# Kernel tuning notes

Measured on AMD Instinct MI355X. Metric: run time of the kernel, lower is better.

The kernel has to match this reference:

```python
import jax, jax.numpy as jnp
import numpy as np
from jax.scipy.special import logsumexp

B, T, D, H, BASIS = 16, 512, 256, 8, 8
E = D // H  # att_emb_size = 32
SINKHORN_ITERS = 20


def setup_inputs() -> dict:
    key = jax.random.key(0)
    ks = jax.random.split(key, 9)
    s = 1.0 / np.sqrt(D)
    return {
        'X': jax.random.normal(ks[0], (B, T, D), jnp.float32),
        'token_embeddings': jax.random.normal(ks[1], (T, D), jnp.float32) * s,
        'Wq_meta': jax.random.normal(ks[2], (T, BASIS, D), jnp.float32) * s,
        'Wk_meta': jax.random.normal(ks[3], (T, BASIS, D), jnp.float32) * s,
        'Q_basis': jax.random.normal(ks[4], (BASIS, D, H * E), jnp.float32) * s,
        'K_basis': jax.random.normal(ks[5], (BASIS, D, H * E), jnp.float32) * s,
        'W_V': jax.random.normal(ks[6], (T, D, H * E), jnp.float32) * s,
        'A_logits': jax.random.normal(ks[7], (T, T), jnp.float32) * 0.05,
        'lambda_logits': jax.random.normal(ks[8], (T, T), jnp.float32) * 0.05,
    }


def log_sinkhorn(log_alpha, n_iters=SINKHORN_ITERS):
    def body(i, la):
        la = la - logsumexp(la, axis=-1, keepdims=True)
        la = la - logsumexp(la, axis=-2, keepdims=True)
        return la
    return jnp.exp(jax.lax.fori_loop(0, n_iters, body, log_alpha))


def reference(X, token_embeddings, Wq_meta, Wk_meta, Q_basis, K_basis, W_V, A_logits, lambda_logits):
    # per-token basis mixing weights: Linear(d,basis) applied to token i's embedding
    q_w = jnp.einsum('td,tkd->tk', token_embeddings, Wq_meta)  # [T, basis]
    k_w = jnp.einsum('td,tkd->tk', token_embeddings, Wk_meta)
    Q_tilde = jnp.einsum('tk,kde->tde', q_w, Q_basis)  # [T, D, H*E]
    K_tilde = jnp.einsum('tk,kde->tde', k_w, K_basis)
    querys = jnp.einsum('btd,tde->bte', X, Q_tilde)  # [B, T, H*E]
    keys = jnp.einsum('btd,tde->bte', X, K_tilde)
    values = jnp.einsum('btd,tde->bte', X, W_V)
    # -> [H, B, T, E]
    q = querys.reshape(B, T, H, E).transpose(2, 0, 1, 3)
    k = keys.reshape(B, T, H, E).transpose(2, 0, 1, 3)
    v = values.reshape(B, T, H, E).transpose(2, 0, 1, 3)
    scores = jnp.einsum('hbte,hbse->hbts', q, k) / np.sqrt(E).astype(np.float32)
    att = jax.nn.softmax(scores, axis=-1)  # dropout=0 (eval)
    lam = jax.nn.sigmoid(lambda_logits)  # [T, T]
    A_sym = 0.5 * (A_logits + A_logits.T)
    att = lam[None, None] * A_sym[None, None] + (1.0 - lam)[None, None] * att
    att = 0.5 * (att + jnp.swapaxes(att, -1, -2))
    att = log_sinkhorn(att)
    out = jnp.einsum('hbts,hbse->hbte', att, v)  # [H, B, T, E]
    return out.transpose(1, 2, 0, 3).reshape(B, T, D)
```

## Files before the change

### kernel.cpp

```cpp
#include <hip/hip_runtime.h>
#include <hip/hip_bf16.h>
#include <stdint.h>


#define B_  16
#define T_  512
#define D_  256
#define H_  8
#define E_  32
#define HE_ 256
#define KB_ 8
#define HB_ 128

typedef unsigned short u16;
typedef __attribute__((ext_vector_type(8))) short short8;
typedef __attribute__((ext_vector_type(4))) float floatx4;

__device__ __forceinline__ float bflo(uint32_t u){ return __uint_as_float(u << 16); }
__device__ __forceinline__ float bfhi(uint32_t u){ return __uint_as_float(u & 0xffff0000u); }
__device__ __forceinline__ u16 f2bf(float f){
  uint32_t u = __float_as_uint(f);
  return (u16)((u + 0x7fffu + ((u >> 16) & 1u)) >> 16);
}
__device__ __forceinline__ uint32_t pk2(float a, float b){
  return (uint32_t)f2bf(a) | ((uint32_t)f2bf(b) << 16);
}

__global__ void __launch_bounds__(256)
kcvt_x(const float* __restrict__ X, u16* __restrict__ Xb){
  int idx = (blockIdx.x*256 + threadIdx.x)*4;
  float4 v = *(const float4*)(X + idx);
  uint2 o; o.x = pk2(v.x, v.y); o.y = pk2(v.z, v.w);
  *(uint2*)(Xb + idx) = o;
}

__global__ void __launch_bounds__(256)
kT_basis(const float* __restrict__ Qb, const float* __restrict__ Kb,
         u16* __restrict__ QbT, u16* __restrict__ KbT){
  __shared__ float tile[64][65];
  int slot = blockIdx.y;
  const float* src = (slot < 8) ? Qb + (size_t)slot*D_*HE_ : Kb + (size_t)(slot-8)*D_*HE_;
  u16*         dst = (slot < 8) ? QbT + (size_t)slot*HE_*D_ : KbT + (size_t)(slot-8)*HE_*D_;
  int ti = blockIdx.x >> 2, tj = blockIdx.x & 3;
  int tid = threadIdx.x;
  #pragma unroll
  for (int i = 0; i < 16; ++i){
    int idx = tid + 256*i;
    int rr = idx >> 6, cc = idx & 63;
    tile[rr][cc] = src[(size_t)(ti*64 + rr)*HE_ + tj*64 + cc];
  }
  __syncthreads();
  #pragma unroll
  for (int i = 0; i < 16; ++i){
    int idx = tid + 256*i;
    int rr = idx >> 6, cc = idx & 63;
    dst[(size_t)(tj*64 + rr)*D_ + ti*64 + cc] = f2bf(tile[cc][rr]);
  }
}

__global__ void k0_meta(const float* __restrict__ te, const float* __restrict__ wq,
                        const float* __restrict__ wk, float* __restrict__ qw,
                        float* __restrict__ kw){
  int t = blockIdx.x;
  int lane = threadIdx.x;
  int k = lane >> 3, part = lane & 7;
  const float* ta = te + t*D_ + part*32;
  const float* qa = wq + (t*KB_ + k)*D_ + part*32;
  const float* ka = wk + (t*KB_ + k)*D_ + part*32;
  float sq = 0.f, sk = 0.f;
  #pragma unroll
  for (int i = 0; i < 8; ++i){
    float4 a = ((const float4*)ta)[i];
    float4 b = ((const float4*)qa)[i];
    float4 c = ((const float4*)ka)[i];
    sq += a.x*b.x + a.y*b.y + a.z*b.z + a.w*b.w;
    sk += a.x*c.x + a.y*c.y + a.z*c.z + a.w*c.w;
  }
  sq += __shfl_down(sq, 4, 8); sq += __shfl_down(sq, 2, 8); sq += __shfl_down(sq, 1, 8);
  sk += __shfl_down(sk, 4, 8); sk += __shfl_down(sk, 2, 8); sk += __shfl_down(sk, 1, 8);
  if (part == 0){
    qw[t*KB_ + k] = sq * 0.17677669529663687f;
    kw[t*KB_ + k] = sk;
  }
}

__global__ void __launch_bounds__(256)
k_pre(const float* __restrict__ A, const float* __restrict__ L,
      u16* __restrict__ lA, u16* __restrict__ oml){
  __shared__ float tile[64][65];
  int I = blockIdx.x >> 3, J = blockIdx.x & 7;
  int tid = threadIdx.x;
  #pragma unroll
  for (int i = 0; i < 16; ++i){
    int idx = tid + 256*i;
    int rr = idx >> 6, cc = idx & 63;
    tile[rr][cc] = A[(J*64 + rr)*T_ + I*64 + cc];
  }
  __syncthreads();
  #pragma unroll
  for (int i = 0; i < 16; ++i){
    int idx = tid + 256*i;
    int rr = idx >> 6, cc = idx & 63;
    int t = I*64 + rr, s = J*64 + cc;
    float lamv = 1.0f / (1.0f + __expf(-L[t*T_ + s]));
    float asym = 0.5f*(A[t*T_ + s] + tile[cc][rr]);
    lA[t*T_ + s]  = f2bf(lamv*asym);
    oml[t*T_ + s] = f2bf(1.0f - lamv);
  }
}

__global__ void __launch_bounds__(256)
k1a_gemm(const u16* __restrict__ Xb, const u16* __restrict__ BT, u16* __restrict__ Y){
  __shared__ u16 At[128*40];
  __shared__ u16 Bt[128*40];
  int bt0 = blockIdx.x*128;
  int j   = blockIdx.y;
  int kb  = blockIdx.z;
  const u16* Bsrc = BT + (size_t)kb*HE_*D_;
  int tid = threadIdx.x, lane = tid & 63, w = tid >> 6;
  int q_l = lane >> 4, c_l = lane & 15;
  int srow = tid >> 2, sch = (tid & 3)*8;
  floatx4 acc[2][8];
  #pragma unroll
  for (int mt = 0; mt < 2; ++mt)
    #pragma unroll
    for (int n = 0; n < 8; ++n) acc[mt][n] = (floatx4){0,0,0,0};

  #pragma unroll 1
  for (int ks = 0; ks < 8; ++ks){
    int k0 = ks*32;
    if (ks) __syncthreads();
    *(short8*)&At[srow*40 + sch] = *(const short8*)&Xb[(size_t)(bt0 + srow)*D_ + k0 + sch];
    *(short8*)&Bt[srow*40 + sch] = *(const short8*)&Bsrc[(size_t)(j*128 + srow)*D_ + k0 + sch];
    __syncthreads();
    short8 a0 = *(const short8*)&At[(w*32 +  0 + c_l)*40 + q_l*8];
    short8 a1 = *(const short8*)&At[(w*32 + 16 + c_l)*40 + q_l*8];
    #pragma unroll
    for (int n = 0; n < 8; ++n){
      short8 bfr = *(const short8*)&Bt[(n*16 + c_l)*40 + q_l*8];
      acc[0][n] = __builtin_amdgcn_mfma_f32_16x16x32_bf16(a0, bfr, acc[0][n], 0, 0, 0);
      acc[1][n] = __builtin_amdgcn_mfma_f32_16x16x32_bf16(a1, bfr, acc[1][n], 0, 0, 0);
    }
  }
  #pragma unroll
  for (int mt = 0; mt < 2; ++mt)
    #pragma unroll
    for (int n = 0; n < 8; ++n)
      #pragma unroll
      for (int r = 0; r < 4; ++r){
        int row = w*32 + mt*16 + q_l*4 + r;
        int e = j*128 + n*16 + c_l;
        Y[((size_t)kb << 21) + (size_t)(bt0 + row)*HE_ + e] = f2bf(acc[mt][n][r]);
      }
}

__global__ void __launch_bounds__(256)
k1b_mix(const u16* __restrict__ Y, const float* __restrict__ wv, u16* __restrict__ dst){
  int tid = threadIdx.x;
  int row = blockIdx.x*16 + (tid >> 4);
  int e0 = (tid & 15)*16;
  int b = row >> 9, t = row & 511;
  float w8[8];
  #pragma unroll
  for (int k = 0; k < 8; ++k) w8[k] = wv[t*8 + k];
  float acc[16];
  #pragma unroll
  for (int i = 0; i < 16; ++i) acc[i] = 0.f;
  #pragma unroll
  for (int k = 0; k < 8; ++k){
    const u16* yp = Y + ((size_t)k << 21) + (size_t)row*HE_ + e0;
    uint4 v0 = *(const uint4*)yp;
    uint4 v1 = *(const uint4*)(yp + 8);
    uint32_t vv[8] = {v0.x,v0.y,v0.z,v0.w,v1.x,v1.y,v1.z,v1.w};
    float wk = w8[k];
    #pragma unroll
    for (int d = 0; d < 8; ++d){
      acc[2*d]   += wk*bflo(vv[d]);
      acc[2*d+1] += wk*bfhi(vv[d]);
    }
  }
  uint4 o0, o1;
  o0.x = pk2(acc[0],acc[1]);   o0.y = pk2(acc[2],acc[3]);
  o0.z = pk2(acc[4],acc[5]);   o0.w = pk2(acc[6],acc[7]);
  o1.x = pk2(acc[8],acc[9]);   o1.y = pk2(acc[10],acc[11]);
  o1.z = pk2(acc[12],acc[13]); o1.w = pk2(acc[14],acc[15]);
  int h = e0 >> 5, off = e0 & 31;
  u16* dp = dst + (((size_t)(h*16 + b)*T_ + t)*E_ + off);
  *(uint4*)dp = o0;
  *(uint4*)(dp + 8) = o1;
}

__global__ void __launch_bounds__(512)
k1c_v(const u16* __restrict__ Xb, const float* __restrict__ WV, u16* __restrict__ v_ws){
  __shared__ u16 lds[128*256];
  int t = blockIdx.x;
  int tid = threadIdx.x;
  int d = tid >> 1, esub = (tid & 1)*64;
  int lane = tid & 63, wv = tid >> 6;
  int q_l = lane >> 4, c_l = lane & 15;
  short8 afrag[8];
  #pragma unroll
  for (int kk = 0; kk < 8; ++kk)
    afrag[kk] = *(const short8*)&Xb[((size_t)c_l*T_ + t)*D_ + kk*32 + q_l*8];
  for (int eh = 0; eh < 2; ++eh){
    #pragma unroll 1
    for (int i = 0; i < 8; ++i){
      int el0 = esub + 8*i;
      int eg0 = eh*128 + el0;
      const float* p = &WV[((size_t)t*D_ + d)*HE_ + eg0];
      float4 m0 = *(const float4*)p;
      float4 m1 = *(const float4*)(p + 4);
      float v[8] = {m0.x,m0.y,m0.z,m0.w,m1.x,m1.y,m1.z,m1.w};
      #pragma unroll
      for (int jj = 0; jj < 8; ++jj){
        int el = el0 + jj;
        lds[el*256 + (((d>>3) ^ (el&31))<<3) + (d&7)] = f2bf(v[jj]);
      }
    }
    __syncthreads();
    floatx4 acc = {0,0,0,0};
    int el = wv*16 + c_l;
    #pragma unroll
    for (int kk = 0; kk < 8; ++kk){
      int c = kk*4 + q_l;
      short8 bfr = *(const short8*)&lds[el*256 + ((c ^ (el&31))<<3)];
      acc = __builtin_amdgcn_mfma_f32_16x16x32_bf16(afrag[kk], bfr, acc, 0, 0, 0);
    }
    int e_full = eh*128 + wv*16 + c_l;
    #pragma unroll
    for (int r = 0; r < 4; ++r){
      int b = q_l*4 + r;
      v_ws[(((size_t)(e_full >> 5)*B_ + b)*T_ + t)*E_ + (e_full & 31)] = f2bf(acc[r]);
    }
    __syncthreads();
  }
}

__global__ void __launch_bounds__(256)
k2a_att(const u16* __restrict__ q_ws, const u16* __restrict__ k_ws,
        const u16* __restrict__ lA, const u16* __restrict__ oml,
        u16* __restrict__ Mc, int hb0){
  int tt = blockIdx.x;
  int hbl = blockIdx.y;
  int hb = hb0 + hbl;
  int tid = threadIdx.x;
  int lane = tid & 63, wv = tid >> 6;
  int q_l = lane >> 4, c_l = lane & 15;
  int t0 = tt*64 + wv*16;
  const u16* qb = q_ws + (size_t)hb*T_*E_;
  const u16* kb = k_ws + (size_t)hb*T_*E_;
  short8 af = *(const short8*)&qb[(t0 + c_l)*E_ + q_l*8];
  floatx4 acc[32];
  #pragma unroll
  for (int st = 0; st < 32; ++st){
    short8 bfr = *(const short8*)&kb[(st*16 + c_l)*E_ + q_l*8];
    floatx4 z = {0,0,0,0};
    acc[st] = __builtin_amdgcn_mfma_f32_16x16x32_bf16(af, bfr, z, 0, 0, 0);
  }
  #pragma unroll
  for (int r = 0; r < 4; ++r){
    float mx = -1e30f;
    #pragma unroll
    for (int st = 0; st < 32; ++st) mx = fmaxf(mx, acc[st][r]);
    mx = fmaxf(mx, __shfl_xor(mx, 1)); mx = fmaxf(mx, __shfl_xor(mx, 2));
    mx = fmaxf(mx, __shfl_xor(mx, 4)); mx = fmaxf(mx, __shfl_xor(mx, 8));
    float sum = 0.f;
    #pragma unroll
    for (int st = 0; st < 32; ++st){ float e = __expf(acc[st][r] - mx); acc[st][r] = e; sum += e; }
    sum += __shfl_xor(sum, 1); sum += __shfl_xor(sum, 2);
    sum += __shfl_xor(sum, 4); sum += __shfl_xor(sum, 8);
    float inv = 1.0f / sum;
    #pragma unroll
    for (int st = 0; st < 32; ++st) acc[st][r] *= inv;
  }
  size_t ob = (size_t)hbl*T_*T_;
  #pragma unroll 1
  for (int st = 0; st < 32; ++st){
    #pragma unroll
    for (int r = 0; r < 4; ++r){
      int t = t0 + q_l*4 + r;
      int s = st*16 + c_l;
      float la = bflo((uint32_t)lA[t*T_ + s]);
      float om = bflo((uint32_t)oml[t*T_ + s]);
      Mc[ob + (size_t)t*T_ + s] = f2bf(la + om*acc[st][r]);
    }
  }
}

__global__ void __launch_bounds__(256)
k2b_sym(u16* __restrict__ Mc){
  __shared__ u16 tA[64][65], tB[64][65];
  int p = blockIdx.x, I = 0;
  while (p >= 8 - I){ p -= 8 - I; ++I; }
  int J = I + p;
  int hbl = blockIdx.y;
  size_t base = (size_t)hbl*T_*T_;
  int tid = threadIdx.x;
  #pragma unroll
  for (int i = 0; i < 16; ++i){
    int idx = tid + 256*i;
    int rr = idx >> 6, cc = idx & 63;
    tA[rr][cc] = Mc[base + (size_t)(I*64 + rr)*T_ + J*64 + cc];
    tB[rr][cc] = Mc[base + (size_t)(J*64 + rr)*T_ + I*64 + cc];
  }
  __syncthreads();
  #pragma unroll
  for (int i = 0; i < 16; ++i){
    int idx = tid + 256*i;
    int rr = idx >> 6, cc = idx & 63;
    float a = bflo((uint32_t)tA[rr][cc]);
    float b = bflo((uint32_t)tB[cc][rr]);
    Mc[base + (size_t)(I*64 + rr)*T_ + J*64 + cc] = f2bf(__expf(0.5f*(a + b)));
  }
  if (I != J){
    #pragma unroll
    for (int i = 0; i < 16; ++i){
      int idx = tid + 256*i;
      int rr = idx >> 6, cc = idx & 63;
      float a = bflo((uint32_t)tB[rr][cc]);
      float b = bflo((uint32_t)tA[cc][rr]);
      Mc[base + (size_t)(J*64 + rr)*T_ + I*64 + cc] = f2bf(__expf(0.5f*(a + b)));
    }
  }
}

#define K3_NREG 92
#define K3_NLDS 36
__global__ void __launch_bounds__(1024)
k3_sinkhorn(const u16* __restrict__ Mc, float* __restrict__ r_ws, float* __restrict__ c_ws,
            int hb0){
  __shared__ uint32_t mlds[K3_NLDS*1024];
  __shared__ float vbuf[512];
  __shared__ float partial[1024];
  int hbl = blockIdx.x;
  int i = threadIdx.x;
  int r = i & 511, h = i >> 9;
  int ch0 = h << 8;
  const uint4* rp = (const uint4*)(Mc + ((size_t)hbl*T_ + r)*T_ + ch0);
  uint4 m4[23];
  #pragma unroll
  for (int j = 0; j < 23; ++j) m4[j] = rp[j];
  #pragma unroll
  for (int j = 0; j < K3_NLDS/4; ++j){
    uint4 v = rp[23 + j];
    mlds[(4*j + 0)*1024 + i] = v.x;
    mlds[(4*j + 1)*1024 + i] = v.y;
    mlds[(4*j + 2)*1024 + i] = v.z;
    mlds[(4*j + 3)*1024 + i] = v.w;
  }
  if (h == 0) vbuf[r] = 1.0f;
  __syncthreads();
  float lr = 0.f, lc = 1.0f;
  #pragma unroll 1
  for (int p = 0; p < 40; ++p){
    float a0 = 0.f, a1 = 0.f, a2 = 0.f, a3 = 0.f;
    #pragma unroll
    for (int q = 0; q < 23; ++q){
      float4 w0 = *(const float4*)&vbuf[ch0 + 8*q];
      float4 w1 = *(const float4*)&vbuf[ch0 + 8*q + 4];
      uint4 x = m4[q];
      a0 += bflo(x.x)*w0.x; a1 += bfhi(x.x)*w0.y;
      a2 += bflo(x.y)*w0.z; a3 += bfhi(x.y)*w0.w;
      a0 += bflo(x.z)*w1.x; a1 += bfhi(x.z)*w1.y;
      a2 += bflo(x.w)*w1.z; a3 += bfhi(x.w)*w1.w;
    }
    #pragma unroll
    for (int j = 0; j < K3_NLDS; j += 2){
      float4 w = *(const float4*)&vbuf[ch0 + 2*K3_NREG + 2*j];
      uint32_t x0 = mlds[j*1024 + i], x1 = mlds[(j+1)*1024 + i];
      a0 += bflo(x0)*w.x; a1 += bfhi(x0)*w.y;
      a2 += bflo(x1)*w.z; a3 += bfhi(x1)*w.w;
    }
    partial[i] = (a0 + a1) + (a2 + a3);
    __syncthreads();
    float nv = 1.0f / (partial[r] + partial[r + 512]);
    if (p & 1) lc = nv; else lr = nv;
    if (h == 0) vbuf[r] = nv;
    __syncthreads();
  }
  if (h == 0){
    int hb = hb0 + hbl;
    r_ws[hb*T_ + r] = lr;
    c_ws[hb*T_ + r] = lc;
  }
}

#define K4_VS 520
__global__ void __launch_bounds__(256)
k4_out(const u16* __restrict__ Mc, const u16* __restrict__ v_ws,
       const float* __restrict__ r_ws, const float* __restrict__ c_ws,
       float* __restrict__ out, int hb0){
  __shared__ u16 vt[32*K4_VS + 8];
  int th = blockIdx.x;
  int hbl = blockIdx.y;
  int hb = hb0 + hbl;
  int h = hb >> 4, b = hb & 15;
  int tid = threadIdx.x;
  const u16* vb = v_ws + (size_t)hb*T_*E_;
  const float* cvec = c_ws + hb*T_;
  #pragma unroll
  for (int rr = 0; rr < 2; ++rr){
    int s = tid + rr*256;
    float cs = cvec[s];
    #pragma unroll
    for (int j4 = 0; j4 < 4; ++j4){
      uint4 v = *(const uint4*)&vb[s*E_ + j4*8];
      uint32_t vv[4] = {v.x,v.y,v.z,v.w};
      #pragma unroll
      for (int j = 0; j < 4; ++j){
        vt[(j4*8 + 2*j    )*K4_VS + s] = f2bf(bflo(vv[j])*cs);
        vt[(j4*8 + 2*j + 1)*K4_VS + s] = f2bf(bfhi(vv[j])*cs);
      }
    }
  }
  __syncthreads();
  int lane = tid & 63, wv = tid >> 6;
  int q_l = lane >> 4, c_l = lane & 15;
  const float* rvec = r_ws + hb*T_;
  const u16* mrow = Mc + (size_t)hbl*T_*T_;
  #pragma unroll 1
  for (int mt = 0; mt < 4; ++mt){
    int t0 = th*256 + (wv*4 + mt)*16;
    floatx4 acc0 = {0,0,0,0}, acc1 = {0,0,0,0};
    #pragma unroll
    for (int kk = 0; kk < 16; ++kk){
      int k0 = kk*32;
      short8 af = *(const short8*)&mrow[(size_t)(t0 + c_l)*T_ + k0 + q_l*8];
      short8 b0 = *(const short8*)&vt[(0  + c_l)*K4_VS + k0 + q_l*8];
      short8 b1 = *(const short8*)&vt[(16 + c_l)*K4_VS + k0 + q_l*8];
      acc0 = __builtin_amdgcn_mfma_f32_16x16x32_bf16(af, b0, acc0, 0, 0, 0);
      acc1 = __builtin_amdgcn_mfma_f32_16x16x32_bf16(af, b1, acc1, 0, 0, 0);
    }
    #pragma unroll
    for (int r = 0; r < 4; ++r){
      int t = t0 + q_l*4 + r;
      float rt = rvec[t];
      out[((size_t)(b*T_ + t))*HE_ + h*E_ + 0  + c_l] = acc0[r]*rt;
      out[((size_t)(b*T_ + t))*HE_ + h*E_ + 16 + c_l] = acc1[r]*rt;
    }
  }
}

extern "C" void kernel_launch(void* const* d_in, const int* in_sizes, int n_in,
                              void* d_out, int out_size, void* d_ws, size_t ws_size,
                              hipStream_t stream){
  const float* X  = (const float*)d_in[0];
  const float* te = (const float*)d_in[1];
  const float* Wq = (const float*)d_in[2];
  const float* Wk = (const float*)d_in[3];
  const float* Qb = (const float*)d_in[4];
  const float* Kb = (const float*)d_in[5];
  const float* WV = (const float*)d_in[6];
  const float* Al = (const float*)d_in[7];
  const float* Ll = (const float*)d_in[8];
  float* out = (float*)d_out;
  (void)in_sizes; (void)n_in; (void)out_size;

  char* w = (char*)d_ws;
  float* qw   = (float*)w;  w += 16384;
  float* kw   = (float*)w;  w += 16384;
  u16* lA     = (u16*)w;    w += 524288;
  u16* oml    = (u16*)w;    w += 524288;
  u16* q_ws   = (u16*)w;    w += 4194304;
  u16* k_ws   = (u16*)w;    w += 4194304;
  u16* v_ws   = (u16*)w;    w += 4194304;
  float* r_ws = (float*)w;  w += 262144;
  float* c_ws = (float*)w;  w += 262144;
  u16* slab = (u16*)w;
  u16* Xb  = slab;
  u16* QbT = slab + 2097152;
  u16* KbT = slab + 2621440;
  u16* Y   = slab + 3145728;
  u16* Mc  = slab;
  size_t fixed = (size_t)(w - (char*)d_ws);
  size_t slabsz = (ws_size > fixed) ? (ws_size - fixed) : 0;
  int nhb = HB_;
  while (nhb > 1 && (size_t)nhb*T_*T_*2 > slabsz) nhb >>= 1;

  kcvt_x  <<<2048, 256, 0, stream>>>(X, Xb);
  kT_basis<<<dim3(16, 16), 256, 0, stream>>>(Qb, Kb, QbT, KbT);
  k0_meta <<<T_, 64, 0, stream>>>(te, Wq, Wk, qw, kw);
  k_pre   <<<64, 256, 0, stream>>>(Al, Ll, lA, oml);
  k1c_v   <<<T_, 512, 0, stream>>>(Xb, WV, v_ws);
  k1a_gemm<<<dim3(64, 2, 8), 256, 0, stream>>>(Xb, QbT, Y);
  k1b_mix <<<512, 256, 0, stream>>>(Y, qw, q_ws);
  k1a_gemm<<<dim3(64, 2, 8), 256, 0, stream>>>(Xb, KbT, Y);
  k1b_mix <<<512, 256, 0, stream>>>(Y, kw, k_ws);
  for (int hb0 = 0; hb0 < HB_; hb0 += nhb){
    k2a_att    <<<dim3(8, nhb), 256, 0, stream>>>(q_ws, k_ws, lA, oml, Mc, hb0);
    k2b_sym    <<<dim3(36, nhb), 256, 0, stream>>>(Mc);
    k3_sinkhorn<<<nhb, 1024, 0, stream>>>(Mc, r_ws, c_ws, hb0);
    k4_out     <<<dim3(2, nhb), 256, 0, stream>>>(Mc, v_ws, r_ws, c_ws, out, hb0);
  }
}
```

Measured before the change: 1.182 ms.

## Split Sinkhorn matrix storage across registers, LDS, and streamed global loads

Each thread's 256-element row slice of the Sinkhorn matrix used to live mostly in registers (184 elements) with the rest in LDS. Now only 72 elements stay in registers and 72 in LDS, while the remaining 112 are re-read from global memory (likely L2-resident) on every one of the 40 passes. This frees registers to reduce spilling or pressure, but adds repeated global/L2 traffic inside the iteration loop.

```diff
diff --git a/kernel.cpp b/kernel.cpp
--- a/kernel.cpp
+++ b/kernel.cpp
@@ -324,12 +324,13 @@
   }
 }
 
-#define K3_NREG 92
-#define K3_NLDS 36
+#define K3_NRQ 9
+#define K3_NLQ 9
+#define K3_NSQ 14
 __global__ void __launch_bounds__(1024)
 k3_sinkhorn(const u16* __restrict__ Mc, float* __restrict__ r_ws, float* __restrict__ c_ws,
             int hb0){
-  __shared__ uint32_t mlds[K3_NLDS*1024];
+  __shared__ uint32_t mlds[K3_NLQ*4*1024];
   __shared__ float vbuf[512];
   __shared__ float partial[1024];
   int hbl = blockIdx.x;
@@ -337,17 +338,18 @@
   int r = i & 511, h = i >> 9;
   int ch0 = h << 8;
   const uint4* rp = (const uint4*)(Mc + ((size_t)hbl*T_ + r)*T_ + ch0);
-  uint4 m4[23];
-  #pragma unroll
-  for (int j = 0; j < 23; ++j) m4[j] = rp[j];
-  #pragma unroll
-  for (int j = 0; j < K3_NLDS/4; ++j){
-    uint4 v = rp[23 + j];
+  uint4 mr[K3_NRQ];
+  #pragma unroll
+  for (int j = 0; j < K3_NRQ; ++j) mr[j] = rp[j];
+  #pragma unroll
+  for (int j = 0; j < K3_NLQ; ++j){
+    uint4 v = rp[K3_NRQ + j];
     mlds[(4*j + 0)*1024 + i] = v.x;
     mlds[(4*j + 1)*1024 + i] = v.y;
     mlds[(4*j + 2)*1024 + i] = v.z;
     mlds[(4*j + 3)*1024 + i] = v.w;
   }
+  const uint4* rps = rp + (K3_NRQ + K3_NLQ);
   if (h == 0) vbuf[r] = 1.0f;
   __syncthreads();
   float lr = 0.f, lc = 1.0f;
@@ -355,21 +357,37 @@
   for (int p = 0; p < 40; ++p){
     float a0 = 0.f, a1 = 0.f, a2 = 0.f, a3 = 0.f;
     #pragma unroll
-    for (int q = 0; q < 23; ++q){
+    for (int q = 0; q < K3_NRQ; ++q){
       float4 w0 = *(const float4*)&vbuf[ch0 + 8*q];
       float4 w1 = *(const float4*)&vbuf[ch0 + 8*q + 4];
-      uint4 x = m4[q];
+      uint4 x = mr[q];
       a0 += bflo(x.x)*w0.x; a1 += bfhi(x.x)*w0.y;
       a2 += bflo(x.y)*w0.z; a3 += bfhi(x.y)*w0.w;
       a0 += bflo(x.z)*w1.x; a1 += bfhi(x.z)*w1.y;
       a2 += bflo(x.w)*w1.z; a3 += bfhi(x.w)*w1.w;
     }
     #pragma unroll
-    for (int j = 0; j < K3_NLDS; j += 2){
-      float4 w = *(const float4*)&vbuf[ch0 + 2*K3_NREG + 2*j];
-      uint32_t x0 = mlds[j*1024 + i], x1 = mlds[(j+1)*1024 + i];
-      a0 += bflo(x0)*w.x; a1 += bfhi(x0)*w.y;
-      a2 += bflo(x1)*w.z; a3 += bfhi(x1)*w.w;
+    for (int q = 0; q < K3_NLQ; ++q){
+      float4 w0 = *(const float4*)&vbuf[ch0 + 72 + 8*q];
+      float4 w1 = *(const float4*)&vbuf[ch0 + 72 + 8*q + 4];
+      uint32_t x0 = mlds[(4*q + 0)*1024 + i];
+      uint32_t x1 = mlds[(4*q + 1)*1024 + i];
+      uint32_t x2 = mlds[(4*q + 2)*1024 + i];
+      uint32_t x3 = mlds[(4*q + 3)*1024 + i];
+      a0 += bflo(x0)*w0.x; a1 += bfhi(x0)*w0.y;
+      a2 += bflo(x1)*w0.z; a3 += bfhi(x1)*w0.w;
+      a0 += bflo(x2)*w1.x; a1 += bfhi(x2)*w1.y;
+      a2 += bflo(x3)*w1.z; a3 += bfhi(x3)*w1.w;
+    }
+    #pragma unroll
+    for (int q = 0; q < K3_NSQ; ++q){
+      uint4 x = rps[q];
+      float4 w0 = *(const float4*)&vbuf[ch0 + 144 + 8*q];
+      float4 w1 = *(const float4*)&vbuf[ch0 + 144 + 8*q + 4];
+      a0 += bflo(x.x)*w0.x; a1 += bfhi(x.x)*w0.y;
+      a2 += bflo(x.y)*w0.z; a3 += bfhi(x.y)*w0.w;
+      a0 += bflo(x.z)*w1.x; a1 += bfhi(x.z)*w1.y;
+      a2 += bflo(x.w)*w1.z; a3 += bfhi(x.w)*w1.w;
     }
     partial[i] = (a0 + a1) + (a2 + a3);
     __syncthreads();
```

Result: slower. 1.221 ms (+3.3%).
